# Kernel optimization log

Measured on AMD Instinct MI355X. Metric: run time of the kernel, lower is better.

## Reference

```python
import jax, jax.numpy as jnp
import numpy as np

LE_LAMBDA = 1e-08


def setup_inputs() -> dict:
    key = jax.random.key(0)
    k1, k2, k3, k4, k5, k6 = jax.random.split(key, 6)
    V, D = 100000, 128
    B, C, NEG, P = 16384, 10, 50, 4096
    return {
        "input_labels": jax.random.randint(k1, (B,), 0, V, dtype=jnp.int64)
        if jax.config.jax_enable_x64 else jax.random.randint(k1, (B,), 0, V, dtype=jnp.int32),
        "pos_labels": jax.random.randint(k2, (B, C), 0, V, dtype=jnp.int32),
        "neg_labels": jax.random.randint(k3, (B, NEG), 0, V, dtype=jnp.int32),
        "hierarchy_pairs": jax.random.randint(k4, (P, 2), 0, V, dtype=jnp.int32),
        "in_embed_w": jax.random.normal(k5, (V, D), dtype=jnp.float32) * (6.0 / (V + D)) ** 0.5,
        "out_embed_w": jax.random.normal(k6, (V, D), dtype=jnp.float32) * (6.0 / (V + D)) ** 0.5,
    }


def reference(input_labels, pos_labels, neg_labels, hierarchy_pairs, in_embed_w, out_embed_w):
    # Skip-gram with negative sampling
    input_emb = in_embed_w[input_labels]          # [B, D]
    pos_emb = out_embed_w[pos_labels]             # [B, C, D]
    neg_emb = out_embed_w[neg_labels]             # [B, NEG, D]

    pos_dot = jnp.einsum("bcd,bd->bc", pos_emb, input_emb)   # [B, C]
    neg_dot = -jnp.einsum("bnd,bd->bn", neg_emb, input_emb)  # [B, NEG]

    log_pos = jax.nn.log_sigmoid(pos_dot).sum(axis=1)  # [B]
    log_neg = jax.nn.log_sigmoid(neg_dot).sum(axis=1)  # [B]
    loss_graph = -(log_pos + log_neg).mean()

    # Vectorized hierarchy L2: sum_p ||E[cat_p] - E[fclass_p]||^2
    cat_emb = in_embed_w[hierarchy_pairs[:, 0]]     # [P, D]
    fclass_emb = in_embed_w[hierarchy_pairs[:, 1]]  # [P, D]
    loss_hierarchy = 0.5 * LE_LAMBDA * jnp.sum((cat_emb - fclass_emb) ** 2)

    return (loss_graph + loss_hierarchy, loss_hierarchy)
```

## Files before the change

### kernel.cpp

```cpp
#include <hip/hip_runtime.h>

#define BATCH 16384
#define NPOS 10
#define NNEG 50
#define DIM 128
#define VOCAB 100000
#define NPAIRS 4096
#define NLBL (NPOS + NNEG)
#define NITER (NLBL / 4)

#define ROW_BLOCKS (BATCH / 4)
#define PAIR_BLOCKS (NPAIRS / 8)
#define CONV_BLOCKS (VOCAB * DIM / 8 / 256)

#define QSCALE     128.0f
#define QINV_SCALE 0.0078125f

typedef __attribute__((ext_vector_type(2))) float f32x2;

#if defined(__has_builtin)
#if __has_builtin(__builtin_amdgcn_cvt_scalef32_pk_f32_fp4) && __has_builtin(__builtin_amdgcn_cvt_scalef32_pk_fp4_f32)
#define HAVE_FP4 1
#endif
#if __has_builtin(__builtin_amdgcn_update_dpp)
#define HAVE_DPP 1
#endif
#endif
#ifndef HAVE_FP4
#define HAVE_FP4 0
#endif
#ifndef HAVE_DPP
#define HAVE_DPP 0
#endif

__device__ __forceinline__ float log_sigmoid_fast(float x) {
    const float L2E = 1.44269504088896340736f;
    const float LN2 = 0.69314718055994530942f;
    float e = __builtin_amdgcn_exp2f(-fabsf(x) * L2E);
    float l = __builtin_amdgcn_logf(1.0f + e);
    return fminf(x, 0.0f) - l * LN2;
}

__device__ __forceinline__ float row_allreduce16(float p) {
#if HAVE_DPP
    p += __int_as_float(__builtin_amdgcn_update_dpp(
            0, __float_as_int(p), 0x128, 0xF, 0xF, true));
    p += __int_as_float(__builtin_amdgcn_update_dpp(
            0, __float_as_int(p), 0x124, 0xF, 0xF, true));
    p += __int_as_float(__builtin_amdgcn_update_dpp(
            0, __float_as_int(p), 0x122, 0xF, 0xF, true));
    p += __int_as_float(__builtin_amdgcn_update_dpp(
            0, __float_as_int(p), 0x121, 0xF, 0xF, true));
#else
    p += __shfl_xor(p, 1);
    p += __shfl_xor(p, 2);
    p += __shfl_xor(p, 4);
    p += __shfl_xor(p, 8);
#endif
    return p;
}


__device__ __forceinline__ void hier_body(
    const int* __restrict__ pairs, const float* __restrict__ in_embed,
    float* __restrict__ hier_partials, float* red, int pair_block)
{
    const int idx = pair_block * 256 + threadIdx.x;
    const int p = idx >> 5;
    const int c = idx & 31;

    const int a  = pairs[p * 2];
    const int bb = pairs[p * 2 + 1];
    const float4 va = reinterpret_cast<const float4*>(in_embed + (size_t)a  * DIM)[c];
    const float4 vb = reinterpret_cast<const float4*>(in_embed + (size_t)bb * DIM)[c];
    const float dx = va.x - vb.x, dy = va.y - vb.y, dz = va.z - vb.z, dw = va.w - vb.w;
    float ss = dx * dx + dy * dy + dz * dz + dw * dw;

    red[threadIdx.x] = ss;
    __syncthreads();
    for (int s2 = 128; s2 > 0; s2 >>= 1) {
        if (threadIdx.x < s2) red[threadIdx.x] += red[threadIdx.x + s2];
        __syncthreads();
    }
    if (threadIdx.x == 0) hier_partials[pair_block] = red[0];
}

#if HAVE_FP4

__global__ __launch_bounds__(256) void convert_hier_kernel(
    const float* __restrict__ in, unsigned* __restrict__ out,
    const int* __restrict__ pairs, const float* __restrict__ in_embed,
    float* __restrict__ hier_partials, unsigned* __restrict__ done_ctr)
{
    if (blockIdx.x < CONV_BLOCKS) {
        if (blockIdx.x == 0 && threadIdx.x == 0) *done_ctr = 0u;
        const int i = blockIdx.x * 256 + threadIdx.x;
        const float4* src = reinterpret_cast<const float4*>(in) + (size_t)i * 2;
        const float4 a = src[0];
        const float4 b = src[1];
        unsigned w = 0;
        w = __builtin_amdgcn_cvt_scalef32_pk_fp4_f32(w, a.x * QSCALE, a.y * QSCALE, 1.0f, 0);
        w = __builtin_amdgcn_cvt_scalef32_pk_fp4_f32(w, a.z * QSCALE, a.w * QSCALE, 1.0f, 1);
        w = __builtin_amdgcn_cvt_scalef32_pk_fp4_f32(w, b.x * QSCALE, b.y * QSCALE, 1.0f, 2);
        w = __builtin_amdgcn_cvt_scalef32_pk_fp4_f32(w, b.z * QSCALE, b.w * QSCALE, 1.0f, 3);
        out[i] = w;
    } else {
        __shared__ float red[256];
        hier_body(pairs, in_embed, hier_partials, red, blockIdx.x - CONV_BLOCKS);
    }
}

__global__ __launch_bounds__(256) void fused_loss_fp4_kernel(
    const int* __restrict__ input_labels,
    const int* __restrict__ pos_labels,
    const int* __restrict__ neg_labels,
    const float* __restrict__ in_embed,
    const unsigned* __restrict__ out4,
    float* __restrict__ block_sums,
    const float* __restrict__ hier_partials,
    unsigned* __restrict__ done_ctr,
    float* __restrict__ out)
{
    __shared__ float red[256];
    __shared__ int is_last;

    {
        const int lane = threadIdx.x & 63;
        const int wave_in_block = threadIdx.x >> 6;
        const int b = blockIdx.x * 4 + wave_in_block;

        const int g  = lane >> 4;
        const int lg = lane & 15;

        int lbls[NITER];
        #pragma unroll
        for (int i = 0; i < NITER; ++i) {
            const int j = i * 4 + g;
            lbls[i] = (j < NPOS) ? pos_labels[b * NPOS + j]
                                 : neg_labels[b * NNEG + (j - NPOS)];
        }

        const int ilbl = input_labels[b];
        const float4* in_row = reinterpret_cast<const float4*>(in_embed + (size_t)ilbl * DIM);
        const float4 x0 = in_row[lg * 2];
        const float4 x1 = in_row[lg * 2 + 1];

        float acc = 0.0f;
        #pragma unroll
        for (int i = 0; i < NITER; ++i) {
            const float s = (i * 4 + g < NPOS) ? 1.0f : -1.0f;

            const unsigned w = out4[(size_t)lbls[i] * (DIM / 8) + lg];

            const f32x2 f0 = __builtin_amdgcn_cvt_scalef32_pk_f32_fp4(w, 1.0f, 0);
            const f32x2 f1 = __builtin_amdgcn_cvt_scalef32_pk_f32_fp4(w, 1.0f, 1);
            const f32x2 f2 = __builtin_amdgcn_cvt_scalef32_pk_f32_fp4(w, 1.0f, 2);
            const f32x2 f3 = __builtin_amdgcn_cvt_scalef32_pk_f32_fp4(w, 1.0f, 3);

            float p = x0.x * f0.x + x0.y * f0.y + x0.z * f1.x + x0.w * f1.y
                    + x1.x * f2.x + x1.y * f2.y + x1.z * f3.x + x1.w * f3.y;

            p = row_allreduce16(p);

            acc += log_sigmoid_fast(s * (p * QINV_SCALE));
        }

        acc += __shfl_xor(acc, 16);
        acc += __shfl_xor(acc, 32);

        if (lane == 0) red[wave_in_block] = acc;
        __syncthreads();
        if (threadIdx.x == 0) {
            block_sums[blockIdx.x] = (red[0] + red[1]) + (red[2] + red[3]);
            __threadfence();
            unsigned old = atomicAdd(done_ctr, 1u);
            is_last = (old == (unsigned)(ROW_BLOCKS - 1)) ? 1 : 0;
        }
        __syncthreads();
    }

    if (!is_last) return;

    float s = 0.0f;
    for (int i = threadIdx.x; i < ROW_BLOCKS; i += 256) s += block_sums[i];
    red[threadIdx.x] = s;
    __syncthreads();
    for (int k = 128; k > 0; k >>= 1) {
        if (threadIdx.x < k) red[threadIdx.x] += red[threadIdx.x + k];
        __syncthreads();
    }
    const float graph_sum = red[0];
    __syncthreads();

    float h = 0.0f;
    for (int i = threadIdx.x; i < PAIR_BLOCKS; i += 256) h += hier_partials[i];
    red[threadIdx.x] = h;
    __syncthreads();
    for (int k = 128; k > 0; k >>= 1) {
        if (threadIdx.x < k) red[threadIdx.x] += red[threadIdx.x + k];
        __syncthreads();
    }

    if (threadIdx.x == 0) {
        const float loss_h = 0.5e-8f * red[0];
        const float loss_g = -(graph_sum / (float)BATCH);
        out[0] = loss_g + loss_h;
        out[1] = loss_h;
    }
}

#endif


__global__ __launch_bounds__(256) void convert_fp8_kernel(
    const float* __restrict__ in, uint2* __restrict__ out)
{
    const int i = blockIdx.x * 256 + threadIdx.x;
    const float4* src = reinterpret_cast<const float4*>(in) + (size_t)i * 2;
    const float4 a = src[0];
    const float4 b = src[1];
    int lo = 0, hi = 0;
    lo = __builtin_amdgcn_cvt_pk_fp8_f32(a.x * QSCALE, a.y * QSCALE, lo, false);
    lo = __builtin_amdgcn_cvt_pk_fp8_f32(a.z * QSCALE, a.w * QSCALE, lo, true);
    hi = __builtin_amdgcn_cvt_pk_fp8_f32(b.x * QSCALE, b.y * QSCALE, hi, false);
    hi = __builtin_amdgcn_cvt_pk_fp8_f32(b.z * QSCALE, b.w * QSCALE, hi, true);
    out[i] = make_uint2((unsigned)lo, (unsigned)hi);
}

__global__ __launch_bounds__(256) void fused_loss_fp8_kernel(
    const int* __restrict__ input_labels,
    const int* __restrict__ pos_labels,
    const int* __restrict__ neg_labels,
    const int* __restrict__ pairs,
    const float* __restrict__ in_embed,
    const unsigned char* __restrict__ out8,
    float* __restrict__ block_sums,
    float* __restrict__ hier_partials)
{
    __shared__ float red[256];

    if (blockIdx.x < ROW_BLOCKS) {
        const int lane = threadIdx.x & 63;
        const int wave_in_block = threadIdx.x >> 6;
        const int b = blockIdx.x * 4 + wave_in_block;
        const int g  = lane >> 4;
        const int lg = lane & 15;

        int lbls[NITER];
        #pragma unroll
        for (int i = 0; i < NITER; ++i) {
            const int j = i * 4 + g;
            lbls[i] = (j < NPOS) ? pos_labels[b * NPOS + j]
                                 : neg_labels[b * NNEG + (j - NPOS)];
        }

        const int ilbl = input_labels[b];
        const float4* in_row = reinterpret_cast<const float4*>(in_embed + (size_t)ilbl * DIM);
        const float4 x0 = in_row[lg * 2];
        const float4 x1 = in_row[lg * 2 + 1];

        float acc = 0.0f;
        #pragma unroll
        for (int i = 0; i < NITER; ++i) {
            const float s = (i * 4 + g < NPOS) ? 1.0f : -1.0f;
            const uint2* e_row = reinterpret_cast<const uint2*>(out8 + (size_t)lbls[i] * DIM);
            const uint2 w = e_row[lg];
            const f32x2 f0 = __builtin_amdgcn_cvt_pk_f32_fp8((int)w.x, false);
            const f32x2 f1 = __builtin_amdgcn_cvt_pk_f32_fp8((int)w.x, true);
            const f32x2 f2 = __builtin_amdgcn_cvt_pk_f32_fp8((int)w.y, false);
            const f32x2 f3 = __builtin_amdgcn_cvt_pk_f32_fp8((int)w.y, true);
            float p = x0.x * f0.x + x0.y * f0.y + x0.z * f1.x + x0.w * f1.y
                    + x1.x * f2.x + x1.y * f2.y + x1.z * f3.x + x1.w * f3.y;
            p = row_allreduce16(p);
            acc += log_sigmoid_fast(s * (p * QINV_SCALE));
        }
        acc += __shfl_xor(acc, 16);
        acc += __shfl_xor(acc, 32);
        if (lane == 0) red[wave_in_block] = acc;
        __syncthreads();
        if (threadIdx.x == 0)
            block_sums[blockIdx.x] = (red[0] + red[1]) + (red[2] + red[3]);
    } else {
        hier_body(pairs, in_embed, hier_partials, red, blockIdx.x - ROW_BLOCKS);
    }
}

__global__ __launch_bounds__(1024) void finalize_kernel(
    const float* __restrict__ block_sums,
    const float* __restrict__ hier_partials,
    float* __restrict__ out)
{
    __shared__ float red[1024];

    float s = 0.0f;
    for (int i = threadIdx.x; i < ROW_BLOCKS; i += 1024) s += block_sums[i];
    red[threadIdx.x] = s;
    __syncthreads();
    for (int k = 512; k > 0; k >>= 1) {
        if (threadIdx.x < k) red[threadIdx.x] += red[threadIdx.x + k];
        __syncthreads();
    }
    const float graph_sum = red[0];
    __syncthreads();

    float h = (threadIdx.x < PAIR_BLOCKS) ? hier_partials[threadIdx.x] : 0.0f;
    red[threadIdx.x] = h;
    __syncthreads();
    for (int k = 512; k > 0; k >>= 1) {
        if (threadIdx.x < k) red[threadIdx.x] += red[threadIdx.x + k];
        __syncthreads();
    }

    if (threadIdx.x == 0) {
        const float loss_h = 0.5e-8f * red[0];
        const float loss_g = -(graph_sum / (float)BATCH);
        out[0] = loss_g + loss_h;
        out[1] = loss_h;
    }
}

extern "C" void kernel_launch(void* const* d_in, const int* in_sizes, int n_in,
                              void* d_out, int out_size, void* d_ws, size_t ws_size,
                              hipStream_t stream) {
    const int*   input_labels = (const int*)d_in[0];
    const int*   pos_labels   = (const int*)d_in[1];
    const int*   neg_labels   = (const int*)d_in[2];
    const int*   pairs        = (const int*)d_in[3];
    const float* in_embed     = (const float*)d_in[4];
    const float* out_embed    = (const float*)d_in[5];
    float* out = (float*)d_out;

#if HAVE_FP4
    const size_t tab4_bytes = (size_t)VOCAB * DIM / 2;
    const size_t need4 = tab4_bytes
                       + (ROW_BLOCKS + PAIR_BLOCKS) * sizeof(float)
                       + sizeof(unsigned);
    if (ws_size >= need4) {
        unsigned* tab4 = (unsigned*)d_ws;
        float* block_sums    = (float*)((char*)d_ws + tab4_bytes);
        float* hier_partials = block_sums + ROW_BLOCKS;
        unsigned* done_ctr   = (unsigned*)(hier_partials + PAIR_BLOCKS);

        convert_hier_kernel<<<CONV_BLOCKS + PAIR_BLOCKS, 256, 0, stream>>>(
            out_embed, tab4, pairs, in_embed, hier_partials, done_ctr);
        fused_loss_fp4_kernel<<<ROW_BLOCKS, 256, 0, stream>>>(
            input_labels, pos_labels, neg_labels, in_embed, tab4,
            block_sums, hier_partials, done_ctr, out);
        return;
    }
#endif
    const size_t tab8_bytes = (size_t)VOCAB * DIM;
    unsigned char* tab8 = (unsigned char*)d_ws;
    float* block_sums    = (float*)(tab8 + tab8_bytes);
    float* hier_partials = block_sums + ROW_BLOCKS;

    convert_fp8_kernel<<<CONV_BLOCKS, 256, 0, stream>>>(out_embed, (uint2*)tab8);
    fused_loss_fp8_kernel<<<ROW_BLOCKS + PAIR_BLOCKS, 256, 0, stream>>>(
        input_labels, pos_labels, neg_labels, pairs, in_embed, tab8,
        block_sums, hier_partials);
    finalize_kernel<<<1, 1024, 0, stream>>>(block_sums, hier_partials, out);
}
```

Before: 36.45 us.

## Use 8-lane groups with coalesced label load and batched fp4 row gathers

The fp4 row kernel now splits each wave into 8 groups of 8 lanes, each lane handling 16 dims with a uint2 load. Labels are read once with one coalesced per-lane load and spread with shuffles. All 8 embedding gathers are issued before compute, and the dequant scale is folded into the input vector. This cuts the loop to 8 iterations, shortens the DPP reduction to 3 steps, and uses packed f32x2 FMAs, at the cost of masked padding work in the last iteration and more registers.

```diff
diff --git a/kernel.cpp b/kernel.cpp
--- a/kernel.cpp
+++ b/kernel.cpp
@@ -7,7 +7,6 @@
 #define VOCAB 100000
 #define NPAIRS 4096
 #define NLBL (NPOS + NNEG)
-#define NITER (NLBL / 4)
 
 #define ROW_BLOCKS (BATCH / 4)
 #define PAIR_BLOCKS (NPAIRS / 8)
@@ -33,29 +32,27 @@
 #define HAVE_DPP 0
 #endif
 
+#define L2E 1.44269504088896340736f
+#define LN2 0.69314718055994530942f
+
 __device__ __forceinline__ float log_sigmoid_fast(float x) {
-    const float L2E = 1.44269504088896340736f;
-    const float LN2 = 0.69314718055994530942f;
     float e = __builtin_amdgcn_exp2f(-fabsf(x) * L2E);
     float l = __builtin_amdgcn_logf(1.0f + e);
     return fminf(x, 0.0f) - l * LN2;
 }
 
-__device__ __forceinline__ float row_allreduce16(float p) {
+__device__ __forceinline__ float allreduce8(float p) {
 #if HAVE_DPP
     p += __int_as_float(__builtin_amdgcn_update_dpp(
-            0, __float_as_int(p), 0x128, 0xF, 0xF, true));
+            0, __float_as_int(p), 0xB1, 0xF, 0xF, true));
     p += __int_as_float(__builtin_amdgcn_update_dpp(
-            0, __float_as_int(p), 0x124, 0xF, 0xF, true));
+            0, __float_as_int(p), 0x4E, 0xF, 0xF, true));
     p += __int_as_float(__builtin_amdgcn_update_dpp(
-            0, __float_as_int(p), 0x122, 0xF, 0xF, true));
-    p += __int_as_float(__builtin_amdgcn_update_dpp(
-            0, __float_as_int(p), 0x121, 0xF, 0xF, true));
+            0, __float_as_int(p), 0x141, 0xF, 0xF, true));
 #else
     p += __shfl_xor(p, 1);
     p += __shfl_xor(p, 2);
     p += __shfl_xor(p, 4);
-    p += __shfl_xor(p, 8);
 #endif
     return p;
 }
@@ -129,42 +126,64 @@
         const int wave_in_block = threadIdx.x >> 6;
         const int b = blockIdx.x * 4 + wave_in_block;
 
-        const int g  = lane >> 4;
-        const int lg = lane & 15;
-
-        int lbls[NITER];
-        #pragma unroll
-        for (int i = 0; i < NITER; ++i) {
-            const int j = i * 4 + g;
-            lbls[i] = (j < NPOS) ? pos_labels[b * NPOS + j]
-                                 : neg_labels[b * NNEG + (j - NPOS)];
-        }
+        const int g8 = lane >> 3;
+        const int l8 = lane & 7;
+
+        const int j0 = lane;
+        int lblv;
+        if (j0 < NPOS)      lblv = pos_labels[b * NPOS + j0];
+        else if (j0 < NLBL) lblv = neg_labels[b * NNEG + (j0 - NPOS)];
+        else                lblv = pos_labels[b * NPOS];
+
+        int lbls[8];
+        #pragma unroll
+        for (int i = 0; i < 8; ++i)
+            lbls[i] = __shfl(lblv, i * 8 + g8);
 
         const int ilbl = input_labels[b];
         const float4* in_row = reinterpret_cast<const float4*>(in_embed + (size_t)ilbl * DIM);
-        const float4 x0 = in_row[lg * 2];
-        const float4 x1 = in_row[lg * 2 + 1];
+        f32x2 xp[8];
+        #pragma unroll
+        for (int k = 0; k < 4; ++k) {
+            const float4 v = in_row[l8 * 4 + k];
+            xp[k * 2]     = f32x2{v.x * QINV_SCALE, v.y * QINV_SCALE};
+            xp[k * 2 + 1] = f32x2{v.z * QINV_SCALE, v.w * QINV_SCALE};
+        }
+
+        const uint2* tab2 = reinterpret_cast<const uint2*>(out4);
+        uint2 w[8];
+        #pragma unroll
+        for (int i = 0; i < 8; ++i)
+            w[i] = tab2[(size_t)lbls[i] * 8 + l8];
 
         float acc = 0.0f;
         #pragma unroll
-        for (int i = 0; i < NITER; ++i) {
-            const float s = (i * 4 + g < NPOS) ? 1.0f : -1.0f;
-
-            const unsigned w = out4[(size_t)lbls[i] * (DIM / 8) + lg];
-
-            const f32x2 f0 = __builtin_amdgcn_cvt_scalef32_pk_f32_fp4(w, 1.0f, 0);
-            const f32x2 f1 = __builtin_amdgcn_cvt_scalef32_pk_f32_fp4(w, 1.0f, 1);
-            const f32x2 f2 = __builtin_amdgcn_cvt_scalef32_pk_f32_fp4(w, 1.0f, 2);
-            const f32x2 f3 = __builtin_amdgcn_cvt_scalef32_pk_f32_fp4(w, 1.0f, 3);
-
-            float p = x0.x * f0.x + x0.y * f0.y + x0.z * f1.x + x0.w * f1.y
-                    + x1.x * f2.x + x1.y * f2.y + x1.z * f3.x + x1.w * f3.y;
-
-            p = row_allreduce16(p);
-
-            acc += log_sigmoid_fast(s * (p * QINV_SCALE));
-        }
-
+        for (int i = 0; i < 8; ++i) {
+            f32x2 d2 = xp[0] * __builtin_amdgcn_cvt_scalef32_pk_f32_fp4(w[i].x, 1.0f, 0);
+            d2 += xp[1] * __builtin_amdgcn_cvt_scalef32_pk_f32_fp4(w[i].x, 1.0f, 1);
+            d2 += xp[2] * __builtin_amdgcn_cvt_scalef32_pk_f32_fp4(w[i].x, 1.0f, 2);
+            d2 += xp[3] * __builtin_amdgcn_cvt_scalef32_pk_f32_fp4(w[i].x, 1.0f, 3);
+            d2 += xp[4] * __builtin_amdgcn_cvt_scalef32_pk_f32_fp4(w[i].y, 1.0f, 0);
+            d2 += xp[5] * __builtin_amdgcn_cvt_scalef32_pk_f32_fp4(w[i].y, 1.0f, 1);
+            d2 += xp[6] * __builtin_amdgcn_cvt_scalef32_pk_f32_fp4(w[i].y, 1.0f, 2);
+            d2 += xp[7] * __builtin_amdgcn_cvt_scalef32_pk_f32_fp4(w[i].y, 1.0f, 3);
+            float p = d2.x + d2.y;
+
+            p = allreduce8(p);
+
+            const float ap = fabsf(p);
+            const float e  = __builtin_amdgcn_exp2f(ap * (-L2E));
+            const float l  = __builtin_amdgcn_logf(1.0f + e);
+            float t;
+            if (i == 0)       t = 0.5f * (p - ap) - LN2 * l;
+            else if (i == 1) { const float sp = (g8 < 2) ? p : -p;
+                               t = 0.5f * (sp - ap) - LN2 * l; }
+            else              t = 0.5f * (-p - ap) - LN2 * l;
+            if (i == 7) t = (g8 < 4) ? t : 0.0f;
+            acc += t;
+        }
+
+        acc += __shfl_xor(acc, 8);
         acc += __shfl_xor(acc, 16);
         acc += __shfl_xor(acc, 32);
 
@@ -246,9 +265,9 @@
         const int g  = lane >> 4;
         const int lg = lane & 15;
 
-        int lbls[NITER];
-        #pragma unroll
-        for (int i = 0; i < NITER; ++i) {
+        int lbls[15];
+        #pragma unroll
+        for (int i = 0; i < 15; ++i) {
             const int j = i * 4 + g;
             lbls[i] = (j < NPOS) ? pos_labels[b * NPOS + j]
                                  : neg_labels[b * NNEG + (j - NPOS)];
@@ -261,7 +280,7 @@
 
         float acc = 0.0f;
         #pragma unroll
-        for (int i = 0; i < NITER; ++i) {
+        for (int i = 0; i < 15; ++i) {
             const float s = (i * 4 + g < NPOS) ? 1.0f : -1.0f;
             const uint2* e_row = reinterpret_cast<const uint2*>(out8 + (size_t)lbls[i] * DIM);
             const uint2 w = e_row[lg];
@@ -271,7 +290,10 @@
             const f32x2 f3 = __builtin_amdgcn_cvt_pk_f32_fp8((int)w.y, true);
             float p = x0.x * f0.x + x0.y * f0.y + x0.z * f1.x + x0.w * f1.y
                     + x1.x * f2.x + x1.y * f2.y + x1.z * f3.x + x1.w * f3.y;
-            p = row_allreduce16(p);
+            p += __shfl_xor(p, 1);
+            p += __shfl_xor(p, 2);
+            p += __shfl_xor(p, 4);
+            p += __shfl_xor(p, 8);
             acc += log_sigmoid_fast(s * (p * QINV_SCALE));
         }
         acc += __shfl_xor(acc, 16);
```

After: 37.30 us. 2.3% more time.
